# Kernel tuning notes

Hardware: AMD Instinct MI355X
Metric: run time of the kernel (lower is better)

## Reference

```python
import jax, jax.numpy as jnp
import numpy as np

B, T, C = 4, 2048, 1024
H, HS = 16, 64


def setup_inputs() -> dict:
    key = jax.random.key(0)
    ks = jax.random.split(key, 5)
    scale = (H * C) ** (-0.5)
    x = jax.random.normal(ks[0], (B, T, C), dtype=jnp.float32)
    Wk = jax.random.normal(ks[1], (H, C, HS), dtype=jnp.float32) * scale
    Wq = jax.random.normal(ks[2], (H, C, HS), dtype=jnp.float32) * scale
    Wv = jax.random.normal(ks[3], (H, C, HS), dtype=jnp.float32) * scale
    proj_w = jax.random.normal(ks[4], (C, C), dtype=jnp.float32) / C ** 0.5
    proj_b = jnp.zeros((C,), dtype=jnp.float32)
    return {"x": x, "Wk": Wk, "Wq": Wq, "Wv": Wv, "proj_w": proj_w, "proj_b": proj_b}


def reference(x, Wk, Wq, Wv, proj_w, proj_b):
    b, t, c = x.shape
    # per-head projections: (B,T,C) x (H,C,D) -> (B,H,T,D)
    q = jnp.einsum('btc,hcd->bhtd', x, Wq)
    k = jnp.einsum('btc,hcd->bhtd', x, Wk)
    v = jnp.einsum('btc,hcd->bhtd', x, Wv)
    # NOTE: original module does not scale by 1/sqrt(head_size)
    wei = jnp.einsum('bhtd,bhsd->bhts', q, k)  # (B,H,T,T)
    causal = jnp.tril(jnp.ones((t, t), dtype=bool))
    wei = jnp.where(causal, wei, -jnp.inf)
    wei = jax.nn.softmax(wei, axis=-1)
    out = jnp.einsum('bhts,bhsd->bhtd', wei, v)
    out = out.transpose(0, 2, 1, 3).reshape(b, t, c)  # concat heads
    return out @ proj_w + proj_b
```

## Files before the change

### kernel.cpp

```cpp
#include <hip/hip_runtime.h>

typedef unsigned short u16;
typedef u16 u16x4 __attribute__((ext_vector_type(4)));
typedef u16 u16x8 __attribute__((ext_vector_type(8)));
typedef unsigned uint2v __attribute__((ext_vector_type(2)));
typedef unsigned uint4v __attribute__((ext_vector_type(4)));
typedef __bf16 bf16x2 __attribute__((ext_vector_type(2)));
typedef __bf16 bf16x8 __attribute__((ext_vector_type(8)));
typedef float f32x4 __attribute__((ext_vector_type(4)));

#define DEV static __device__ __forceinline__

DEV u16 f2bf(float f) {
  union { float f; unsigned u; } v; v.f = f;
  return (u16)((v.u + 0x7FFFu + ((v.u >> 16) & 1u)) >> 16);
}

DEV void async16(const void* g, void* l) {
  __builtin_amdgcn_global_load_lds((const __attribute__((address_space(1))) void*)g,
                                   (__attribute__((address_space(3))) void*)l, 16, 0, 0);
}

DEV f32x4 mfma16(bf16x8 a, bf16x8 b, f32x4 c) {
  return __builtin_amdgcn_mfma_f32_16x16x32_bf16(a, b, c, 0, 0, 0);
}

DEV float exp2fast(float x) { return __builtin_amdgcn_exp2f(x); }

#define BARRIER() asm volatile("s_barrier" ::: "memory")
#define SB0() __builtin_amdgcn_sched_barrier(0)

__global__ __launch_bounds__(256) void k_prep(const float* __restrict__ x,
                                              const float* __restrict__ Wk,
                                              const float* __restrict__ Wq,
                                              const float* __restrict__ Wv,
                                              const float* __restrict__ pw,
                                              u16* __restrict__ xb,
                                              u16* __restrict__ wT,
                                              u16* __restrict__ pwT) {
  __shared__ float t[64 * 72];
  const int bid = blockIdx.x, tid = threadIdx.x;
  if (bid < 8192) {
    int i = bid * 1024 + tid * 4;
    float4 v = *(const float4*)(x + i);
    u16x4 o = { f2bf(v.x), f2bf(v.y), f2bf(v.z), f2bf(v.w) };
    *(u16x4*)(xb + i) = o;
    return;
  }
  const int role = bid - 8192;
  const float* src;
  u16* dst;
  int rows, cols, bx, by, bz;
  float scale;
  if (role < 768) {
    const int w = role >> 8, rem = role & 255;
    src = (w == 0) ? Wq : ((w == 1) ? Wk : Wv);
    dst = wT + (size_t)w * 1024 * 1024;
    scale = (w == 0) ? 1.44269504088896340736f : 1.0f;
    rows = 1024; cols = 64; bx = 0; by = rem >> 4; bz = rem & 15;
  } else {
    const int p = role - 768;
    src = pw; dst = pwT; scale = 1.0f;
    rows = 1024; cols = 1024; bx = p & 15; by = p >> 4; bz = 0;
  }
  src += (size_t)bz * rows * cols;
  dst += (size_t)bz * rows * cols;
  const int c0 = bx * 64, r0 = by * 64;
  const int rr = tid >> 2, cb = (tid & 3) * 16;
  const float* s = src + (size_t)(r0 + rr) * cols + c0 + cb;
  float4 v0 = *(const float4*)(s + 0);
  float4 v1 = *(const float4*)(s + 4);
  float4 v2 = *(const float4*)(s + 8);
  float4 v3 = *(const float4*)(s + 12);
  *(float4*)(t + rr * 72 + cb + 0)  = v0;
  *(float4*)(t + rr * 72 + cb + 4)  = v1;
  *(float4*)(t + rr * 72 + cb + 8)  = v2;
  *(float4*)(t + rr * 72 + cb + 12) = v3;
  __syncthreads();
  const int dd = tid >> 2, eb = (tid & 3) * 16;
  u16x8 o0, o1;
#pragma unroll
  for (int e = 0; e < 8; ++e) o0[e] = f2bf(t[(eb + e) * 72 + dd] * scale);
#pragma unroll
  for (int e = 0; e < 8; ++e) o1[e] = f2bf(t[(eb + 8 + e) * 72 + dd] * scale);
  u16* dp = dst + (size_t)(c0 + dd) * rows + r0 + eb;
  *(u16x8*)dp = o0;
  *(u16x8*)(dp + 8) = o1;
}

template <int MODE>
__global__ __launch_bounds__(512, 2) void k_gemm(const u16* __restrict__ A,
                                                 const u16* __restrict__ Bt,
                                                 u16* __restrict__ qd,
                                                 u16* __restrict__ kd,
                                                 u16* __restrict__ vd,
                                                 float* __restrict__ out,
                                                 const float* __restrict__ bias) {
  constexpr int BN   = (MODE == 0) ? 192 : 128;
  constexpr int AI   = (MODE == 0) ? 8 : 4;
  constexpr int AJ   = (MODE == 0) ? 3 : 4;
  constexpr int GB   = BN / 64;
  constexpr int GXC  = (MODE == 0) ? 16 : 8;
  constexpr int SLOT = (256 + BN) * 64;
  constexpr int RING = (MODE == 0) ? 2 : 3;
  __shared__ u16 lds[RING * SLOT];

  const int tid = threadIdx.x;
  const int w = tid >> 6, lane = tid & 63;
  const int quad = lane >> 4, l15 = lane & 15;
  const int wm = (MODE == 0) ? (w >> 2) : (w >> 1);
  const int wn = (MODE == 0) ? (w & 3) : (w & 1);

  constexpr int NWG = GXC * 32;
  int lin = (int)blockIdx.y * GXC + (int)blockIdx.x;
  lin = (lin & 7) * (NWG >> 3) + (lin >> 3);
  const size_t mb = (size_t)(lin / GXC);
  const int nb = lin % GXC;

  const int lr = lane >> 3;
  const int lc = ((lane & 7) ^ lr) << 3;
  const u16* ga0 = A  + (mb * 256 + (size_t)(w * 8 + lr)) * 1024 + lc;
  const u16* gb0 = Bt + ((size_t)nb * BN + (size_t)(w * 8 + lr)) * 1024 + lc;

  const int swz0 = ((0 + quad) ^ (l15 & 7)) << 3;
  const int swz1 = ((4 + quad) ^ (l15 & 7)) << 3;

  f32x4 acc[AI][AJ] = {};

  if constexpr (MODE == 0) {
    {
      u16* sb = lds + w * 512;
#pragma unroll
      for (int g = 0; g < 4; ++g) async16(ga0 + (size_t)g * 65536, sb + g * 4096);
#pragma unroll
      for (int g = 0; g < GB; ++g) async16(gb0 + (size_t)g * 65536, sb + 16384 + g * 4096);
    }
    asm volatile("s_waitcnt vmcnt(0)" ::: "memory");
    BARRIER(); SB0();

    for (int s = 0; s < 16; ++s) {
      const u16* Ab = lds + (s & 1) * SLOT;
      const u16* Bb = Ab + 16384;
      u16* nsb = lds + ((s + 1) & 1) * SLOT + w * 512;
      const int ko = (s + 1) * 64;

      bf16x8 a0[AI], b0[AJ];
#pragma unroll
      for (int i = 0; i < AI; ++i)
        a0[i] = *(const bf16x8*)(Ab + (wm * (AI * 16) + i * 16 + l15) * 64 + swz0);
#pragma unroll
      for (int j = 0; j < AJ; ++j)
        b0[j] = *(const bf16x8*)(Bb + (wn * (AJ * 16) + j * 16 + l15) * 64 + swz0);
      if (s < 15) {
#pragma unroll
        for (int g = 0; g < 4; ++g)
          async16(ga0 + (size_t)g * 65536 + ko, nsb + g * 4096);
      }
      SB0(); BARRIER(); SB0();
      __builtin_amdgcn_s_setprio(1);
#pragma unroll
      for (int i = 0; i < AI; ++i)
#pragma unroll
        for (int j = 0; j < AJ; ++j) acc[i][j] = mfma16(a0[i], b0[j], acc[i][j]);
      __builtin_amdgcn_s_setprio(0);
      SB0(); BARRIER(); SB0();

      bf16x8 a1[AI], b1[AJ];
#pragma unroll
      for (int i = 0; i < AI; ++i)
        a1[i] = *(const bf16x8*)(Ab + (wm * (AI * 16) + i * 16 + l15) * 64 + swz1);
#pragma unroll
      for (int j = 0; j < AJ; ++j)
        b1[j] = *(const bf16x8*)(Bb + (wn * (AJ * 16) + j * 16 + l15) * 64 + swz1);
      if (s < 15) {
#pragma unroll
        for (int g = 0; g < GB; ++g)
          async16(gb0 + (size_t)g * 65536 + ko, nsb + 16384 + g * 4096);
      }
      SB0(); BARRIER(); SB0();
      __builtin_amdgcn_s_setprio(1);
#pragma unroll
      for (int i = 0; i < AI; ++i)
#pragma unroll
        for (int j = 0; j < AJ; ++j) acc[i][j] = mfma16(a1[i], b1[j], acc[i][j]);
      __builtin_amdgcn_s_setprio(0);
      SB0();
      if (s < 15) {
        asm volatile("s_waitcnt vmcnt(0) lgkmcnt(0)" ::: "memory");
        BARRIER(); SB0();
      }
    }
  } else {
    auto STAGE = [&](int buf, int s) {
      u16* sb = lds + buf * SLOT + w * 512;
      const int ko = s * 64;
#pragma unroll
      for (int g = 0; g < 4; ++g)
        async16(ga0 + (size_t)g * 65536 + ko, sb + g * 4096);
#pragma unroll
      for (int g = 0; g < GB; ++g)
        async16(gb0 + (size_t)g * 65536 + ko, sb + 16384 + g * 4096);
    };
    STAGE(0, 0);
    STAGE(1, 1);
    asm volatile("s_waitcnt vmcnt(6)" ::: "memory");
    BARRIER(); SB0();

    for (int s = 0; s < 16; ++s) {
      const u16* Ab = lds + (s % 3) * SLOT;
      const u16* Bb = Ab + 16384;

      bf16x8 a0[AI], b0[AJ];
#pragma unroll
      for (int i = 0; i < AI; ++i)
        a0[i] = *(const bf16x8*)(Ab + (wm * (AI * 16) + i * 16 + l15) * 64 + swz0);
#pragma unroll
      for (int j = 0; j < AJ; ++j)
        b0[j] = *(const bf16x8*)(Bb + (wn * (AJ * 16) + j * 16 + l15) * 64 + swz0);
      if (s < 14) {
        u16* d = lds + ((s + 2) % 3) * SLOT + w * 512;
        async16(ga0 + 0 * 65536 + (s + 2) * 64, d + 0 * 4096);
        async16(ga0 + 1 * 65536 + (s + 2) * 64, d + 1 * 4096);
        async16(ga0 + 2 * 65536 + (s + 2) * 64, d + 2 * 4096);
      }
      SB0(); BARRIER(); SB0();
      __builtin_amdgcn_s_setprio(1);
#pragma unroll
      for (int i = 0; i < AI; ++i)
#pragma unroll
        for (int j = 0; j < AJ; ++j) acc[i][j] = mfma16(a0[i], b0[j], acc[i][j]);
      __builtin_amdgcn_s_setprio(0);
      SB0(); BARRIER(); SB0();

      bf16x8 a1[AI], b1[AJ];
#pragma unroll
      for (int i = 0; i < AI; ++i)
        a1[i] = *(const bf16x8*)(Ab + (wm * (AI * 16) + i * 16 + l15) * 64 + swz1);
#pragma unroll
      for (int j = 0; j < AJ; ++j)
        b1[j] = *(const bf16x8*)(Bb + (wn * (AJ * 16) + j * 16 + l15) * 64 + swz1);
      if (s < 14) {
        u16* d = lds + ((s + 2) % 3) * SLOT + w * 512;
        async16(ga0 + 3 * 65536 + (s + 2) * 64, d + 3 * 4096);
        async16(gb0 + 0 * 65536 + (s + 2) * 64, d + 16384 + 0 * 4096);
        async16(gb0 + 1 * 65536 + (s + 2) * 64, d + 16384 + 4096);
      }
      SB0(); BARRIER(); SB0();
      __builtin_amdgcn_s_setprio(1);
#pragma unroll
      for (int i = 0; i < AI; ++i)
#pragma unroll
        for (int j = 0; j < AJ; ++j) acc[i][j] = mfma16(a1[i], b1[j], acc[i][j]);
      __builtin_amdgcn_s_setprio(0);
      SB0();
      if (s < 14)       { asm volatile("s_waitcnt vmcnt(6)" ::: "memory"); }
      else if (s == 14) { asm volatile("s_waitcnt vmcnt(0)" ::: "memory"); }
      if (s < 15) { BARRIER(); SB0(); }
    }
  }

  const size_t m0 = mb * 256 + wm * (AI * 16);
  const int n0 = nb * BN + wn * (AJ * 16);
  if (MODE == 0) {
#pragma unroll
    for (int j = 0; j < AJ; ++j) {
      const int n = n0 + j * 16 + l15;
      const int p = n >> 10, hh = (n >> 6) & 15, d = n & 63;
      if (p == 2) {
#pragma unroll
        for (int i = 0; i < AI; ++i) {
          const size_t m = m0 + i * 16 + quad * 4;
          const size_t bb = m >> 11, tt = m & 2047;
          u16x4 pk = { f2bf(acc[i][j][0]), f2bf(acc[i][j][1]),
                       f2bf(acc[i][j][2]), f2bf(acc[i][j][3]) };
          *(u16x4*)(vd + ((bb * 16 + hh) * 64 + d) * 2048 + tt) = pk;
        }
      } else {
        u16* dst = (p == 0) ? qd : kd;
#pragma unroll
        for (int i = 0; i < AI; ++i)
#pragma unroll
          for (int r = 0; r < 4; ++r) {
            const size_t m = m0 + i * 16 + quad * 4 + r;
            const size_t bb = m >> 11, tt = m & 2047;
            dst[((bb * 16 + hh) * 2048 + tt) * 64 + d] = f2bf(acc[i][j][r]);
          }
      }
    }
  } else {
#pragma unroll
    for (int j = 0; j < AJ; ++j) {
      const int n = n0 + j * 16 + l15;
      const float bv = bias[n];
#pragma unroll
      for (int i = 0; i < AI; ++i)
#pragma unroll
        for (int r = 0; r < 4; ++r) {
          const size_t m = m0 + i * 16 + quad * 4 + r;
          out[m * 1024 + n] = acc[i][j][r] + bv;
        }
    }
  }
}

__global__ __launch_bounds__(256) void k_attn(const u16* __restrict__ Qg,
                                              const u16* __restrict__ Kg,
                                              const u16* __restrict__ Vtg,
                                              u16* __restrict__ Og) {
  __shared__ u16 Kbuf[2 * 4096];
  __shared__ u16 Vbuf[2 * 4096];
  const int tid = threadIdx.x;
  const int wave = tid >> 6, lane = tid & 63;
  const int quad = lane >> 4, l15 = lane & 15;
  const int quad4 = quad * 4, quad8 = quad * 8;
  const int bh = blockIdx.x;
  const int qb = 15 - (int)blockIdx.y;
  const u16* kg = Kg + (size_t)bh * 2048 * 64;
  const u16* vg = Vtg + (size_t)bh * 64 * 2048;
  const int b = bh >> 4, h = bh & 15;

  const int lrow = lane >> 3;
  const int lchunk = ((lane & 7) ^ lrow) << 3;
  const u16* kst = kg + (size_t)(wave * 16 + lrow) * 64 + lchunk;
  const u16* vst = vg + (size_t)(wave * 16 + lrow) * 2048 + lchunk;
  u16* kdst0 = Kbuf + wave * 1024;
  u16* vdst0 = Vbuf + wave * 1024;

  const int rowoff = l15 * 64;
  const int swz0 = ((0 + quad) ^ (l15 & 7)) << 3;
  const int swz1 = ((4 + quad) ^ (l15 & 7)) << 3;

  const int qlo = qb * 128 + wave * 32;
  const int ntw = 2 * qb + 1 + (wave >> 1);
  const int ntb = 2 * qb + 2;
  const u16* qg = Qg + ((size_t)bh * 2048 + (size_t)qb * 128) * 64;

  bf16x8 qf[2][2];
#pragma unroll
  for (int i = 0; i < 2; ++i)
#pragma unroll
    for (int c = 0; c < 2; ++c)
      qf[i][c] = *(const bf16x8*)(qg + (size_t)(wave * 32 + i * 16 + l15) * 64 +
                                  c * 32 + quad8);

  f32x4 oacc[2][4] = {};
  f32x4 lacc[2] = {};
  const f32x4 fzero = {};
  const u16x8 onesu = {0x3F80, 0x3F80, 0x3F80, 0x3F80,
                       0x3F80, 0x3F80, 0x3F80, 0x3F80};
  const bf16x8 onesf = __builtin_bit_cast(bf16x8, onesu);

  async16(kst, kdst0);
  async16(kst + 512, kdst0 + 512);
  async16(vst, vdst0);
  async16(vst + 16384, vdst0 + 512);

  for (int it = 0; it < ntb; ++it) {
    __syncthreads();

    if (it + 1 < ntb) {
      const int buf = (it + 1) & 1;
      const size_t s0n = (size_t)(it + 1) * 64;
      async16(kst + s0n * 64,       kdst0 + buf * 4096);
      async16(kst + s0n * 64 + 512, kdst0 + buf * 4096 + 512);
      async16(vst + s0n,            vdst0 + buf * 4096);
      async16(vst + s0n + 16384,    vdst0 + buf * 4096 + 512);
    }

    if (it < ntw) {
      const int s0 = it * 64;
      const u16* Kb = Kbuf + (it & 1) * 4096;
      const u16* Vb = Vbuf + (it & 1) * 4096;

      f32x4 sacc[4][2];
      __builtin_amdgcn_s_setprio(1);
#pragma unroll
      for (int j = 0; j < 4; ++j) {
        bf16x8 kf0 = *(const bf16x8*)(Kb + j * 1024 + rowoff + swz0);
        bf16x8 kf1 = *(const bf16x8*)(Kb + j * 1024 + rowoff + swz1);
        sacc[j][0] = mfma16(kf0, qf[0][0], fzero);
        sacc[j][0] = mfma16(kf1, qf[0][1], sacc[j][0]);
        sacc[j][1] = mfma16(kf0, qf[1][0], fzero);
        sacc[j][1] = mfma16(kf1, qf[1][1], sacc[j][1]);
      }
      __builtin_amdgcn_s_setprio(0);

#pragma unroll
      for (int j = 0; j < 4; ++j)
#pragma unroll
        for (int i = 0; i < 2; ++i)
#pragma unroll
          for (int r = 0; r < 4; ++r)
            sacc[j][i][r] = exp2fast(sacc[j][i][r]);

      if (it == ntw - 1) {
#pragma unroll
        for (int j = 0; j < 4; ++j)
#pragma unroll
        for (int i = 0; i < 2; ++i)
#pragma unroll
          for (int r = 0; r < 4; ++r)
            if (s0 + j * 16 + quad4 + r > qlo + i * 16 + l15) sacc[j][i][r] = 0.f;
      }

      bf16x8 pa[2][2];
#pragma unroll
      for (int i = 0; i < 2; ++i) {
        unsigned P[8];
#pragma unroll
        for (int j = 0; j < 4; ++j) {
          bf16x2 lo = { (__bf16)sacc[j][i][0], (__bf16)sacc[j][i][1] };
          bf16x2 hi = { (__bf16)sacc[j][i][2], (__bf16)sacc[j][i][3] };
          P[j * 2 + 0] = __builtin_bit_cast(unsigned, lo);
          P[j * 2 + 1] = __builtin_bit_cast(unsigned, hi);
        }
        unsigned wd[8];
#pragma unroll
        for (int g = 0; g < 4; ++g) {
          const int x = (g & 2) * 2 + (g & 1);
          uint2v t = __builtin_amdgcn_permlane32_swap(P[x], P[x + 2], false, false);
          uint2v u = __builtin_amdgcn_permlane16_swap(t.x, t.y, false, false);
          wd[x] = u.x;
          wd[x + 2] = u.y;
        }
        uint4v lo4 = { wd[0], wd[1], wd[2], wd[3] };
        uint4v hi4 = { wd[4], wd[5], wd[6], wd[7] };
        pa[i][0] = __builtin_bit_cast(bf16x8, lo4);
        pa[i][1] = __builtin_bit_cast(bf16x8, hi4);
      }

      __builtin_amdgcn_s_setprio(1);
#pragma unroll
      for (int n = 0; n < 4; ++n) {
        bf16x8 vf0 = *(const bf16x8*)(Vb + n * 1024 + rowoff + swz0);
        bf16x8 vf1 = *(const bf16x8*)(Vb + n * 1024 + rowoff + swz1);
        oacc[0][n] = mfma16(pa[0][0], vf0, oacc[0][n]);
        oacc[0][n] = mfma16(pa[0][1], vf1, oacc[0][n]);
        oacc[1][n] = mfma16(pa[1][0], vf0, oacc[1][n]);
        oacc[1][n] = mfma16(pa[1][1], vf1, oacc[1][n]);
      }
      lacc[0] = mfma16(pa[0][0], onesf, lacc[0]);
      lacc[0] = mfma16(pa[0][1], onesf, lacc[0]);
      lacc[1] = mfma16(pa[1][0], onesf, lacc[1]);
      lacc[1] = mfma16(pa[1][1], onesf, lacc[1]);
      __builtin_amdgcn_s_setprio(0);
    }
  }

#pragma unroll
  for (int i = 0; i < 2; ++i)
#pragma unroll
    for (int r = 0; r < 4; ++r) {
      const float inv = 1.0f / lacc[i][r];
      const size_t t = (size_t)qb * 128 + wave * 32 + i * 16 + quad4 + r;
#pragma unroll
      for (int n = 0; n < 4; ++n)
        Og[((size_t)b * 2048 + t) * 1024 + h * 64 + n * 16 + l15] =
            f2bf(oacc[i][n][r] * inv);
    }
}

extern "C" void kernel_launch(void* const* d_in, const int* in_sizes, int n_in,
                              void* d_out, int out_size, void* d_ws, size_t ws_size,
                              hipStream_t stream) {
  const float* x  = (const float*)d_in[0];
  const float* Wk = (const float*)d_in[1];
  const float* Wq = (const float*)d_in[2];
  const float* Wv = (const float*)d_in[3];
  const float* pw = (const float*)d_in[4];
  const float* pb = (const float*)d_in[5];
  float* out = (float*)d_out;
  char* ws = (char*)d_ws;

  u16* xb  = (u16*)(ws + 0);
  u16* wT  = (u16*)(ws + 16777216);
  u16* pwT = (u16*)(ws + 23068672);
  u16* q   = (u16*)(ws + 25165824);
  u16* kb  = (u16*)(ws + 41943040);
  u16* vt  = (u16*)(ws + 58720256);
  u16* att = (u16*)(ws + 0);

  k_prep<<<9216, 256, 0, stream>>>(x, Wk, Wq, Wv, pw, xb, wT, pwT);
  k_gemm<0><<<dim3(16, 32), 512, 0, stream>>>(xb, wT, q, kb, vt, nullptr, nullptr);
  k_attn<<<dim3(64, 16), 256, 0, stream>>>(q, kb, vt, att);
  k_gemm<1><<<dim3(8, 32), 512, 0, stream>>>(att, pwT, nullptr, nullptr, nullptr, out, pb);
}
```

Before: 231.4 us.

## Load K/V fragments directly from global memory instead of LDS staging

The attention kernel drops the double-buffered LDS staging of K and V tiles, along with the per-iteration __syncthreads. Each wave now reads its K and V MFMA fragments straight from global memory (through the cache), and the V loads are issued before the exp/pack phase to hide latency. This removes barrier coupling between waves with different trip counts and frees LDS. In exchange, every wave reloads the shared K/V tiles redundantly from L2/L1 with less coalesced 16-byte accesses, which adds global memory traffic and latency.

```diff
diff --git a/kernel.cpp b/kernel.cpp
--- a/kernel.cpp
+++ b/kernel.cpp
@@ -307,8 +307,6 @@
                                               const u16* __restrict__ Kg,
                                               const u16* __restrict__ Vtg,
                                               u16* __restrict__ Og) {
-  __shared__ u16 Kbuf[2 * 4096];
-  __shared__ u16 Vbuf[2 * 4096];
   const int tid = threadIdx.x;
   const int wave = tid >> 6, lane = tid & 63;
   const int quad = lane >> 4, l15 = lane & 15;
@@ -319,20 +317,8 @@
   const u16* vg = Vtg + (size_t)bh * 64 * 2048;
   const int b = bh >> 4, h = bh & 15;
 
-  const int lrow = lane >> 3;
-  const int lchunk = ((lane & 7) ^ lrow) << 3;
-  const u16* kst = kg + (size_t)(wave * 16 + lrow) * 64 + lchunk;
-  const u16* vst = vg + (size_t)(wave * 16 + lrow) * 2048 + lchunk;
-  u16* kdst0 = Kbuf + wave * 1024;
-  u16* vdst0 = Vbuf + wave * 1024;
-
-  const int rowoff = l15 * 64;
-  const int swz0 = ((0 + quad) ^ (l15 & 7)) << 3;
-  const int swz1 = ((4 + quad) ^ (l15 & 7)) << 3;
-
   const int qlo = qb * 128 + wave * 32;
   const int ntw = 2 * qb + 1 + (wave >> 1);
-  const int ntb = 2 * qb + 2;
   const u16* qg = Qg + ((size_t)bh * 2048 + (size_t)qb * 128) * 64;
 
   bf16x8 qf[2][2];
@@ -342,6 +328,9 @@
     for (int c = 0; c < 2; ++c)
       qf[i][c] = *(const bf16x8*)(qg + (size_t)(wave * 32 + i * 16 + l15) * 64 +
                                   c * 32 + quad8);
+
+  const u16* kfp = kg + (size_t)l15 * 64 + quad8;
+  const u16* vfp = vg + (size_t)l15 * 2048 + quad8;
 
   f32x4 oacc[2][4] = {};
   f32x4 lacc[2] = {};
@@ -350,101 +339,93 @@
                        0x3F80, 0x3F80, 0x3F80, 0x3F80};
   const bf16x8 onesf = __builtin_bit_cast(bf16x8, onesu);
 
-  async16(kst, kdst0);
-  async16(kst + 512, kdst0 + 512);
-  async16(vst, vdst0);
-  async16(vst + 16384, vdst0 + 512);
-
-  for (int it = 0; it < ntb; ++it) {
-    __syncthreads();
-
-    if (it + 1 < ntb) {
-      const int buf = (it + 1) & 1;
-      const size_t s0n = (size_t)(it + 1) * 64;
-      async16(kst + s0n * 64,       kdst0 + buf * 4096);
-      async16(kst + s0n * 64 + 512, kdst0 + buf * 4096 + 512);
-      async16(vst + s0n,            vdst0 + buf * 4096);
-      async16(vst + s0n + 16384,    vdst0 + buf * 4096 + 512);
-    }
-
-    if (it < ntw) {
-      const int s0 = it * 64;
-      const u16* Kb = Kbuf + (it & 1) * 4096;
-      const u16* Vb = Vbuf + (it & 1) * 4096;
-
-      f32x4 sacc[4][2];
-      __builtin_amdgcn_s_setprio(1);
+  for (int it = 0; it < ntw; ++it) {
+    const int s0 = it * 64;
+
+    bf16x8 kf0[4], kf1[4];
+#pragma unroll
+    for (int j = 0; j < 4; ++j) {
+      const u16* kp = kfp + (size_t)(s0 + j * 16) * 64;
+      kf0[j] = *(const bf16x8*)(kp);
+      kf1[j] = *(const bf16x8*)(kp + 32);
+    }
+
+    f32x4 sacc[4][2];
+    __builtin_amdgcn_s_setprio(1);
+#pragma unroll
+    for (int j = 0; j < 4; ++j) {
+      sacc[j][0] = mfma16(kf0[j], qf[0][0], fzero);
+      sacc[j][0] = mfma16(kf1[j], qf[0][1], sacc[j][0]);
+      sacc[j][1] = mfma16(kf0[j], qf[1][0], fzero);
+      sacc[j][1] = mfma16(kf1[j], qf[1][1], sacc[j][1]);
+    }
+    __builtin_amdgcn_s_setprio(0);
+
+    bf16x8 vf0[4], vf1[4];
+#pragma unroll
+    for (int n = 0; n < 4; ++n) {
+      const u16* vp = vfp + (size_t)(n * 16) * 2048 + s0;
+      vf0[n] = *(const bf16x8*)(vp);
+      vf1[n] = *(const bf16x8*)(vp + 32);
+    }
+
+#pragma unroll
+    for (int j = 0; j < 4; ++j)
+#pragma unroll
+      for (int i = 0; i < 2; ++i)
+#pragma unroll
+        for (int r = 0; r < 4; ++r)
+          sacc[j][i][r] = exp2fast(sacc[j][i][r]);
+
+    if (it == ntw - 1) {
+#pragma unroll
+      for (int j = 0; j < 4; ++j)
+#pragma unroll
+      for (int i = 0; i < 2; ++i)
+#pragma unroll
+        for (int r = 0; r < 4; ++r)
+          if (s0 + j * 16 + quad4 + r > qlo + i * 16 + l15) sacc[j][i][r] = 0.f;
+    }
+
+    bf16x8 pa[2][2];
+#pragma unroll
+    for (int i = 0; i < 2; ++i) {
+      unsigned P[8];
 #pragma unroll
       for (int j = 0; j < 4; ++j) {
-        bf16x8 kf0 = *(const bf16x8*)(Kb + j * 1024 + rowoff + swz0);
-        bf16x8 kf1 = *(const bf16x8*)(Kb + j * 1024 + rowoff + swz1);
-        sacc[j][0] = mfma16(kf0, qf[0][0], fzero);
-        sacc[j][0] = mfma16(kf1, qf[0][1], sacc[j][0]);
-        sacc[j][1] = mfma16(kf0, qf[1][0], fzero);
-        sacc[j][1] = mfma16(kf1, qf[1][1], sacc[j][1]);
-      }
-      __builtin_amdgcn_s_setprio(0);
-
-#pragma unroll
-      for (int j = 0; j < 4; ++j)
-#pragma unroll
-        for (int i = 0; i < 2; ++i)
-#pragma unroll
-          for (int r = 0; r < 4; ++r)
-            sacc[j][i][r] = exp2fast(sacc[j][i][r]);
-
-      if (it == ntw - 1) {
-#pragma unroll
-        for (int j = 0; j < 4; ++j)
-#pragma unroll
-        for (int i = 0; i < 2; ++i)
-#pragma unroll
-          for (int r = 0; r < 4; ++r)
-            if (s0 + j * 16 + quad4 + r > qlo + i * 16 + l15) sacc[j][i][r] = 0.f;
-      }
-
-      bf16x8 pa[2][2];
-#pragma unroll
-      for (int i = 0; i < 2; ++i) {
-        unsigned P[8];
-#pragma unroll
-        for (int j = 0; j < 4; ++j) {
-          bf16x2 lo = { (__bf16)sacc[j][i][0], (__bf16)sacc[j][i][1] };
-          bf16x2 hi = { (__bf16)sacc[j][i][2], (__bf16)sacc[j][i][3] };
-          P[j * 2 + 0] = __builtin_bit_cast(unsigned, lo);
-          P[j * 2 + 1] = __builtin_bit_cast(unsigned, hi);
-        }
-        unsigned wd[8];
-#pragma unroll
-        for (int g = 0; g < 4; ++g) {
-          const int x = (g & 2) * 2 + (g & 1);
-          uint2v t = __builtin_amdgcn_permlane32_swap(P[x], P[x + 2], false, false);
-          uint2v u = __builtin_amdgcn_permlane16_swap(t.x, t.y, false, false);
-          wd[x] = u.x;
-          wd[x + 2] = u.y;
-        }
-        uint4v lo4 = { wd[0], wd[1], wd[2], wd[3] };
-        uint4v hi4 = { wd[4], wd[5], wd[6], wd[7] };
-        pa[i][0] = __builtin_bit_cast(bf16x8, lo4);
-        pa[i][1] = __builtin_bit_cast(bf16x8, hi4);
-      }
-
-      __builtin_amdgcn_s_setprio(1);
-#pragma unroll
-      for (int n = 0; n < 4; ++n) {
-        bf16x8 vf0 = *(const bf16x8*)(Vb + n * 1024 + rowoff + swz0);
-        bf16x8 vf1 = *(const bf16x8*)(Vb + n * 1024 + rowoff + swz1);
-        oacc[0][n] = mfma16(pa[0][0], vf0, oacc[0][n]);
-        oacc[0][n] = mfma16(pa[0][1], vf1, oacc[0][n]);
-        oacc[1][n] = mfma16(pa[1][0], vf0, oacc[1][n]);
-        oacc[1][n] = mfma16(pa[1][1], vf1, oacc[1][n]);
-      }
-      lacc[0] = mfma16(pa[0][0], onesf, lacc[0]);
-      lacc[0] = mfma16(pa[0][1], onesf, lacc[0]);
-      lacc[1] = mfma16(pa[1][0], onesf, lacc[1]);
-      lacc[1] = mfma16(pa[1][1], onesf, lacc[1]);
-      __builtin_amdgcn_s_setprio(0);
-    }
+        bf16x2 lo = { (__bf16)sacc[j][i][0], (__bf16)sacc[j][i][1] };
+        bf16x2 hi = { (__bf16)sacc[j][i][2], (__bf16)sacc[j][i][3] };
+        P[j * 2 + 0] = __builtin_bit_cast(unsigned, lo);
+        P[j * 2 + 1] = __builtin_bit_cast(unsigned, hi);
+      }
+      unsigned wd[8];
+#pragma unroll
+      for (int g = 0; g < 4; ++g) {
+        const int x = (g & 2) * 2 + (g & 1);
+        uint2v t = __builtin_amdgcn_permlane32_swap(P[x], P[x + 2], false, false);
+        uint2v u = __builtin_amdgcn_permlane16_swap(t.x, t.y, false, false);
+        wd[x] = u.x;
+        wd[x + 2] = u.y;
+      }
+      uint4v lo4 = { wd[0], wd[1], wd[2], wd[3] };
+      uint4v hi4 = { wd[4], wd[5], wd[6], wd[7] };
+      pa[i][0] = __builtin_bit_cast(bf16x8, lo4);
+      pa[i][1] = __builtin_bit_cast(bf16x8, hi4);
+    }
+
+    __builtin_amdgcn_s_setprio(1);
+#pragma unroll
+    for (int n = 0; n < 4; ++n) {
+      oacc[0][n] = mfma16(pa[0][0], vf0[n], oacc[0][n]);
+      oacc[0][n] = mfma16(pa[0][1], vf1[n], oacc[0][n]);
+      oacc[1][n] = mfma16(pa[1][0], vf0[n], oacc[1][n]);
+      oacc[1][n] = mfma16(pa[1][1], vf1[n], oacc[1][n]);
+    }
+    lacc[0] = mfma16(pa[0][0], onesf, lacc[0]);
+    lacc[0] = mfma16(pa[0][1], onesf, lacc[0]);
+    lacc[1] = mfma16(pa[1][0], onesf, lacc[1]);
+    lacc[1] = mfma16(pa[1][1], onesf, lacc[1]);
+    __builtin_amdgcn_s_setprio(0);
   }
 
 #pragma unroll
```

Result: slower. 295.8 us (+27.8%).
